# Optimization experiments

Measured on AMD Instinct MI355X. Metric: run time of the kernel, lower is better.

Reference implementation:

```python
import jax, jax.numpy as jnp
import numpy as np

THRESHOLD = 1.0
CURRENT_DECAY = 0.3
VOLTAGE_DECAY = 0.25
TAU_GRAD = 0.001  # surrogate-gradient sharpness (SLAYER escape-rate style)


@jax.custom_vjp
def spike(v):
    return (v >= THRESHOLD).astype(v.dtype)


def _spike_fwd(v):
    return spike(v), v


def _spike_bwd(v, g):
    # SLAYER-style surrogate: dS/dv = exp(-|v - theta| / tau) / tau
    return (g * jnp.exp(-jnp.abs(v - THRESHOLD) / TAU_GRAD) / TAU_GRAD,)


spike.defvjp(_spike_fwd, _spike_bwd)


def weight_norm(v, g):
    # torch weight_norm(dim=0): w = g * v / ||v|| with norm over all non-output dims
    axes = tuple(range(1, v.ndim))
    n = jnp.sqrt(jnp.sum(v * v, axis=axes, keepdims=True))
    return g.reshape((-1,) + (1,) * (v.ndim - 1)) * v / n


def cuba(z):
    # CUBA LIF dynamics over trailing time axis.  z: (B, ..., T)
    zt = jnp.moveaxis(z, -1, 0)  # (T, B, ...)

    def step(carry, z_t):
        c, v = carry
        c = (1.0 - CURRENT_DECAY) * c + z_t
        v = (1.0 - VOLTAGE_DECAY) * v + c
        s = spike(v)
        v = v * (1.0 - s)  # hard reset to zero on spike
        return (c, v), s

    init = (jnp.zeros_like(zt[0]), jnp.zeros_like(zt[0]))
    _, s = jax.lax.scan(step, init, zt)
    return jnp.moveaxis(s, 0, -1)  # (B, ..., T)


def conv2d_t(x, w):
    # Apply 2D conv independently per timestep. x: (B,C,H,W,T), w: (O,I,5,5)
    B, C, H, W, T = x.shape
    xb = jnp.moveaxis(x, -1, 1).reshape(B * T, C, H, W)
    y = jax.lax.conv_general_dilated(
        xb, w, window_strides=(4, 4), padding=[(1, 1), (1, 1)],
        dimension_numbers=('NCHW', 'OIHW', 'NCHW'))
    O, Ho, Wo = y.shape[1], y.shape[2], y.shape[3]
    return jnp.moveaxis(y.reshape(B, T, O, Ho, Wo), 1, -1)  # (B,O,Ho,Wo,T)


def dense_t(x, w):
    # x: (B, I, T), w: (O, I)
    return jnp.einsum('bit,oi->bot', x, w)


def setup_inputs() -> dict:
    key = jax.random.key(0)
    ks = jax.random.split(key, 8)
    B, T = 16, 64
    # sparse binary event input (DVS-like spikes)
    x = (jax.random.uniform(ks[0], (B, 2, 128, 128, T)) < 0.2).astype(jnp.float32)

    def mk(k, shape):
        fan_in = int(np.prod(shape[1:]))
        return jax.random.normal(k, shape, jnp.float32) / np.sqrt(fan_in)

    # weight_norm direction v; gain g absorbs weight_scale=2 (||w_eff|| = 2 per filter)
    return {
        'x': x,
        'conv1_v': mk(ks[1], (8, 2, 5, 5)),   'conv1_g': jnp.full((8,), 2.0, jnp.float32),
        'conv2_v': mk(ks[2], (32, 8, 5, 5)),  'conv2_g': jnp.full((32,), 2.0, jnp.float32),
        'conv3_v': mk(ks[3], (64, 32, 5, 5)), 'conv3_g': jnp.full((64,), 2.0, jnp.float32),
        'dense1_v': mk(ks[4], (2056, 256)),   'dense1_g': jnp.full((2056,), 2.0, jnp.float32),
        'dense2_v': mk(ks[5], (11, 2056)),    'dense2_g': jnp.full((11,), 2.0, jnp.float32),
    }


def reference(x, conv1_v, conv1_g, conv2_v, conv2_g, conv3_v, conv3_g,
              dense1_v, dense1_g, dense2_v, dense2_g):
    B = x.shape[0]
    T = x.shape[-1]
    # conv blocks: synapse then CUBA neuron
    for v, g in ((conv1_v, conv1_g), (conv2_v, conv2_g), (conv3_v, conv3_g)):
        x = cuba(conv2d_t(x, weight_norm(v, g)))
    # flatten (C,H,W) -> features; (B,64,2,2,T) -> (B,256,T)
    x = x.reshape(B, 64 * 2 * 2, T)
    for v, g in ((dense1_v, dense1_g), (dense2_v, dense2_g)):
        x = cuba(dense_t(x, weight_norm(v, g)))
    return x  # (B, 11, T) output spike train
```

## Files before the change

kernel.cpp:

```cpp
#include <hip/hip_runtime.h>
#include <cstddef>

#define TT 64

#define RFL(x) __builtin_amdgcn_readfirstlane(x)

__device__ __forceinline__ void scanc(float& c, float& v, float& z) {
    c = fmaf(0.7f, c, z);
    v = fmaf(0.75f, v, c);
    float s = (v >= 1.0f) ? 1.0f : 0.0f;
    v = (v >= 1.0f) ? 0.0f : v;
    z = s;
}
__device__ __forceinline__ void scan4(float& c, float& v, float4& a) {
    scanc(c, v, a.x); scanc(c, v, a.y); scanc(c, v, a.z); scanc(c, v, a.w);
}

__global__ __launch_bounds__(256) void wnorm_all(
    const float* __restrict__ c1v, const float* __restrict__ c1g, float* __restrict__ w1T,
    const float* __restrict__ c2v, const float* __restrict__ c2g, float* __restrict__ w2T,
    const float* __restrict__ c3v, const float* __restrict__ c3g, float* __restrict__ w3T,
    const float* __restrict__ d1v, const float* __restrict__ d1g, float* __restrict__ wd1,
    const float* __restrict__ d2v, const float* __restrict__ d2g, float* __restrict__ wd2P) {
    __shared__ float red[256];
    const int bid = blockIdx.x;
    const float *v, *g; float* w; int o, K, LD; bool tr;
    if (bid < 8)         { v = c1v; g = c1g; w = w1T;  o = bid;        K = 50;   LD = 8;  tr = true;  }
    else if (bid < 40)   { v = c2v; g = c2g; w = w2T;  o = bid - 8;    K = 200;  LD = 32; tr = true;  }
    else if (bid < 104)  { v = c3v; g = c3g; w = w3T;  o = bid - 40;   K = 800;  LD = 64; tr = true;  }
    else if (bid < 2160) { v = d1v; g = d1g; w = wd1;  o = bid - 104;  K = 256;  LD = 0;  tr = false; }
    else                 { v = d2v; g = d2g; w = wd2P; o = bid - 2160; K = 2056; LD = 12; tr = true;  }

    float s = 0.f;
    for (int k = threadIdx.x; k < K; k += 256) {
        float x = v[(size_t)o * K + k];
        s += x * x;
    }
    red[threadIdx.x] = s;
    __syncthreads();
    for (int off = 128; off > 0; off >>= 1) {
        if (threadIdx.x < off) red[threadIdx.x] += red[threadIdx.x + off];
        __syncthreads();
    }
    const float scale = g[o] / sqrtf(red[0]);
    for (int k = threadIdx.x; k < K; k += 256) {
        float val = scale * v[(size_t)o * K + k];
        if (tr) w[(size_t)k * LD + o] = val;
        else    w[(size_t)o * K + k] = val;
    }
}

__global__ __launch_bounds__(256) void conv1_cuba(const float* __restrict__ x,
                                                  const float* __restrict__ w1T,
                                                  float* __restrict__ s1) {
    __shared__ float lds[4][8][68];
    const int wid = RFL(threadIdx.x >> 6), t = threadIdx.x & 63;
    const int task = RFL(blockIdx.x) * 4 + wid;
    const int spi = task & 1023, b = task >> 10;
    const int oy = spi >> 5, ox = spi & 31;

    float a0=0,a1=0,a2=0,a3=0,a4=0,a5=0,a6=0,a7=0;
    const float* xb = x + (size_t)b * 2 * 128 * 128 * TT + t;

    if (oy >= 1 && ox >= 1) {
        const float* xq = xb + ((size_t)((oy * 4 - 1) * 128 + ox * 4 - 1)) * TT;
        float xv[50];
#pragma unroll
        for (int ci = 0; ci < 2; ci++)
#pragma unroll
            for (int ky = 0; ky < 5; ky++)
#pragma unroll
                for (int kx = 0; kx < 5; kx++)
                    xv[ci * 25 + ky * 5 + kx] =
                        xq[((size_t)(ci * 16384 + ky * 128 + kx)) * TT];
#pragma unroll
        for (int k = 0; k < 50; k++) {
            const float4* wp = (const float4*)(w1T + k * 8);
            const float4 wA = wp[0], wB = wp[1];
            const float xvk = xv[k];
            a0 = fmaf(wA.x, xvk, a0); a1 = fmaf(wA.y, xvk, a1);
            a2 = fmaf(wA.z, xvk, a2); a3 = fmaf(wA.w, xvk, a3);
            a4 = fmaf(wB.x, xvk, a4); a5 = fmaf(wB.y, xvk, a5);
            a6 = fmaf(wB.z, xvk, a6); a7 = fmaf(wB.w, xvk, a7);
        }
    } else {
        for (int ci = 0; ci < 2; ci++) {
#pragma unroll
            for (int ky = 0; ky < 5; ky++) {
                const int iy = oy * 4 + ky - 1;
                if (iy < 0 || iy >= 128) continue;
#pragma unroll
                for (int kx = 0; kx < 5; kx++) {
                    const int ix = ox * 4 + kx - 1;
                    if (ix < 0 || ix >= 128) continue;
                    const float xvk = xb[((size_t)((ci * 128 + iy) * 128 + ix)) * TT];
                    const float4* wp = (const float4*)(w1T + (ci * 25 + ky * 5 + kx) * 8);
                    const float4 wA = wp[0], wB = wp[1];
                    a0 = fmaf(wA.x, xvk, a0); a1 = fmaf(wA.y, xvk, a1);
                    a2 = fmaf(wA.z, xvk, a2); a3 = fmaf(wA.w, xvk, a3);
                    a4 = fmaf(wB.x, xvk, a4); a5 = fmaf(wB.y, xvk, a5);
                    a6 = fmaf(wB.z, xvk, a6); a7 = fmaf(wB.w, xvk, a7);
                }
            }
        }
    }
    lds[wid][0][t] = a0; lds[wid][1][t] = a1; lds[wid][2][t] = a2; lds[wid][3][t] = a3;
    lds[wid][4][t] = a4; lds[wid][5][t] = a5; lds[wid][6][t] = a6; lds[wid][7][t] = a7;
    __syncthreads();
    if (t < 8) {
        const float* row = &lds[wid][t][0];
        float4* op = (float4*)(s1 + (((size_t)b * 8 + t) * 1024 + spi) * TT);
        float c = 0.f, v = 0.f;
        for (int tc = 0; tc < 4; tc++) {
            float4 r0 = *(const float4*)&row[tc * 16 + 0];
            float4 r1 = *(const float4*)&row[tc * 16 + 4];
            float4 r2 = *(const float4*)&row[tc * 16 + 8];
            float4 r3 = *(const float4*)&row[tc * 16 + 12];
            scan4(c, v, r0); scan4(c, v, r1); scan4(c, v, r2); scan4(c, v, r3);
            op[tc * 4 + 0] = r0; op[tc * 4 + 1] = r1;
            op[tc * 4 + 2] = r2; op[tc * 4 + 3] = r3;
        }
    }
}

__global__ __launch_bounds__(256) void conv2_cuba(const float* __restrict__ s1,
                                                  const float* __restrict__ w2T,
                                                  float* __restrict__ s2) {
    __shared__ float lds[4][16][68];
    const int wid = RFL(threadIdx.x >> 6), t = threadIdx.x & 63;
    const int task = RFL(blockIdx.x) * 4 + wid;
    const int og = task & 1;
    const int spi = (task >> 1) & 63;
    const int b = task >> 7;
    const int oy = spi >> 3, ox = spi & 7;

    float a[16];
#pragma unroll
    for (int j = 0; j < 16; j++) a[j] = 0.f;
    const float* xb = s1 + (size_t)b * 8 * 32 * 32 * TT + t;

    if (oy >= 1 && ox >= 1) {
        const float* xq = xb + ((size_t)((oy * 4 - 1) * 32 + ox * 4 - 1)) * TT;
        for (int cp = 0; cp < 4; cp++) {
            float xv[50];
#pragma unroll
            for (int cc = 0; cc < 2; cc++)
#pragma unroll
                for (int ky = 0; ky < 5; ky++)
#pragma unroll
                    for (int kx = 0; kx < 5; kx++)
                        xv[cc * 25 + ky * 5 + kx] =
                            xq[((size_t)(((cp * 2 + cc) * 1024) + ky * 32 + kx)) * TT];
#pragma unroll
            for (int k = 0; k < 50; k++) {
                const int row = (cp * 2 + (k >= 25 ? 1 : 0)) * 25 + (k >= 25 ? k - 25 : k);
                const float4* wp = (const float4*)(w2T + row * 32 + og * 16);
                const float4 w0 = wp[0], w1 = wp[1], w2 = wp[2], w3 = wp[3];
                const float xvk = xv[k];
                a[0]  = fmaf(w0.x, xvk, a[0]);  a[1]  = fmaf(w0.y, xvk, a[1]);
                a[2]  = fmaf(w0.z, xvk, a[2]);  a[3]  = fmaf(w0.w, xvk, a[3]);
                a[4]  = fmaf(w1.x, xvk, a[4]);  a[5]  = fmaf(w1.y, xvk, a[5]);
                a[6]  = fmaf(w1.z, xvk, a[6]);  a[7]  = fmaf(w1.w, xvk, a[7]);
                a[8]  = fmaf(w2.x, xvk, a[8]);  a[9]  = fmaf(w2.y, xvk, a[9]);
                a[10] = fmaf(w2.z, xvk, a[10]); a[11] = fmaf(w2.w, xvk, a[11]);
                a[12] = fmaf(w3.x, xvk, a[12]); a[13] = fmaf(w3.y, xvk, a[13]);
                a[14] = fmaf(w3.z, xvk, a[14]); a[15] = fmaf(w3.w, xvk, a[15]);
            }
        }
    } else {
        for (int ci = 0; ci < 8; ci++) {
#pragma unroll
            for (int ky = 0; ky < 5; ky++) {
                const int iy = oy * 4 + ky - 1;
                if (iy < 0 || iy >= 32) continue;
#pragma unroll
                for (int kx = 0; kx < 5; kx++) {
                    const int ix = ox * 4 + kx - 1;
                    if (ix < 0 || ix >= 32) continue;
                    const float xvk = xb[((size_t)((ci * 32 + iy) * 32 + ix)) * TT];
                    const float4* wp =
                        (const float4*)(w2T + (ci * 25 + ky * 5 + kx) * 32 + og * 16);
                    const float4 w0 = wp[0], w1 = wp[1], w2 = wp[2], w3 = wp[3];
                    a[0]  = fmaf(w0.x, xvk, a[0]);  a[1]  = fmaf(w0.y, xvk, a[1]);
                    a[2]  = fmaf(w0.z, xvk, a[2]);  a[3]  = fmaf(w0.w, xvk, a[3]);
                    a[4]  = fmaf(w1.x, xvk, a[4]);  a[5]  = fmaf(w1.y, xvk, a[5]);
                    a[6]  = fmaf(w1.z, xvk, a[6]);  a[7]  = fmaf(w1.w, xvk, a[7]);
                    a[8]  = fmaf(w2.x, xvk, a[8]);  a[9]  = fmaf(w2.y, xvk, a[9]);
                    a[10] = fmaf(w2.z, xvk, a[10]); a[11] = fmaf(w2.w, xvk, a[11]);
                    a[12] = fmaf(w3.x, xvk, a[12]); a[13] = fmaf(w3.y, xvk, a[13]);
                    a[14] = fmaf(w3.z, xvk, a[14]); a[15] = fmaf(w3.w, xvk, a[15]);
                }
            }
        }
    }
#pragma unroll
    for (int j = 0; j < 16; j++) lds[wid][j][t] = a[j];
    __syncthreads();
    if (t < 16) {
        const float* row = &lds[wid][t][0];
        float4* op = (float4*)(s2 + (((size_t)b * 32 + og * 16 + t) * 64 + spi) * TT);
        float c = 0.f, v = 0.f;
        for (int tc = 0; tc < 4; tc++) {
            float4 r0 = *(const float4*)&row[tc * 16 + 0];
            float4 r1 = *(const float4*)&row[tc * 16 + 4];
            float4 r2 = *(const float4*)&row[tc * 16 + 8];
            float4 r3 = *(const float4*)&row[tc * 16 + 12];
            scan4(c, v, r0); scan4(c, v, r1); scan4(c, v, r2); scan4(c, v, r3);
            op[tc * 4 + 0] = r0; op[tc * 4 + 1] = r1;
            op[tc * 4 + 2] = r2; op[tc * 4 + 3] = r3;
        }
    }
}

template <int OY, int OX>
__device__ __forceinline__ void conv3_acc(const float* __restrict__ xb,
                                          const float* __restrict__ wTo,
                                          int wid, float* __restrict__ acc) {
    constexpr int KY0 = (OY == 0) ? 1 : 0;
    constexpr int KX0 = (OX == 0) ? 1 : 0;
    constexpr int NKY = 5 - KY0;
    constexpr int NKX = 5 - KX0;
    for (int c8 = 0; c8 < 8; c8++) {
        const int ci = wid * 8 + c8;
        float xv[NKY * NKX];
#pragma unroll
        for (int ky = KY0; ky < 5; ky++) {
#pragma unroll
            for (int kx = KX0; kx < 5; kx++) {
                const int iy = OY * 4 + ky - 1;
                const int ix = OX * 4 + kx - 1;
                xv[(ky - KY0) * NKX + (kx - KX0)] =
                    xb[((size_t)((ci * 8 + iy) * 8 + ix)) * TT];
            }
        }
#pragma unroll
        for (int ky = KY0; ky < 5; ky++) {
#pragma unroll
            for (int kx = KX0; kx < 5; kx++) {
                const float xvk = xv[(ky - KY0) * NKX + (kx - KX0)];
                const float4* wp = (const float4*)(wTo + (ci * 25 + ky * 5 + kx) * 64);
                const float4 wA = wp[0], wB = wp[1];
                acc[0] = fmaf(wA.x, xvk, acc[0]); acc[1] = fmaf(wA.y, xvk, acc[1]);
                acc[2] = fmaf(wA.z, xvk, acc[2]); acc[3] = fmaf(wA.w, xvk, acc[3]);
                acc[4] = fmaf(wB.x, xvk, acc[4]); acc[5] = fmaf(wB.y, xvk, acc[5]);
                acc[6] = fmaf(wB.z, xvk, acc[6]); acc[7] = fmaf(wB.w, xvk, acc[7]);
            }
        }
    }
}

__global__ __launch_bounds__(256) void conv3_cuba(const float* __restrict__ s2,
                                                  const float* __restrict__ wT,
                                                  float* __restrict__ s3) {
    __shared__ float red[4][8][68];
    const int wid = RFL(threadIdx.x >> 6), t = threadIdx.x & 63;
    const int og = RFL(blockIdx.x) & 7;
    const int spi = (RFL(blockIdx.x) >> 3) & 3;
    const int b = RFL(blockIdx.x) >> 5;

    float acc[8];
#pragma unroll
    for (int j = 0; j < 8; j++) acc[j] = 0.f;
    const float* xb = s2 + (size_t)b * 32 * 8 * 8 * TT + t;
    const float* wTo = wT + og * 8;

    switch (spi) {
        case 0: conv3_acc<0, 0>(xb, wTo, wid, acc); break;
        case 1: conv3_acc<0, 1>(xb, wTo, wid, acc); break;
        case 2: conv3_acc<1, 0>(xb, wTo, wid, acc); break;
        default: conv3_acc<1, 1>(xb, wTo, wid, acc); break;
    }
#pragma unroll
    for (int j = 0; j < 8; j++) red[wid][j][t] = acc[j];
    __syncthreads();
    if (wid == 0) {
#pragma unroll
        for (int j = 0; j < 8; j++)
            red[0][j][t] = ((red[0][j][t] + red[1][j][t]) + red[2][j][t]) + red[3][j][t];
    }
    __syncthreads();
    if (threadIdx.x < 8) {
        const int j = threadIdx.x;
        const float* row = &red[0][j][0];
        float4* op = (float4*)(s3 + ((size_t)b * 256 + og * 32 + j * 4 + spi) * TT);
        float c = 0.f, v = 0.f;
        for (int tc = 0; tc < 4; tc++) {
            float4 r0 = *(const float4*)&row[tc * 16 + 0];
            float4 r1 = *(const float4*)&row[tc * 16 + 4];
            float4 r2 = *(const float4*)&row[tc * 16 + 8];
            float4 r3 = *(const float4*)&row[tc * 16 + 12];
            scan4(c, v, r0); scan4(c, v, r1); scan4(c, v, r2); scan4(c, v, r3);
            op[tc * 4 + 0] = r0; op[tc * 4 + 1] = r1;
            op[tc * 4 + 2] = r2; op[tc * 4 + 3] = r3;
        }
    }
}

__global__ __launch_bounds__(256) void dense1_cuba(const float* __restrict__ s3,
                                                   const float* __restrict__ w,
                                                   float* __restrict__ s4) {
    __shared__ float lds[4][8][68];
    const int wid = threadIdx.x >> 6, t = threadIdx.x & 63;
    const int task = blockIdx.x * 4 + wid;
    const int bq = task / 257;
    const int ogq = task - bq * 257;
    const int b = RFL(bq);
    const int o0 = RFL(ogq * 8);

    float a0=0,a1=0,a2=0,a3=0,a4=0,a5=0,a6=0,a7=0;
    const float* ab = s3 + (size_t)b * 256 * TT + t;
    const float* r0 = w + (size_t)(o0 + 0) * 256;
    const float* r1 = w + (size_t)(o0 + 1) * 256;
    const float* r2 = w + (size_t)(o0 + 2) * 256;
    const float* r3 = w + (size_t)(o0 + 3) * 256;
    const float* r4 = w + (size_t)(o0 + 4) * 256;
    const float* r5 = w + (size_t)(o0 + 5) * 256;
    const float* r6 = w + (size_t)(o0 + 6) * 256;
    const float* r7 = w + (size_t)(o0 + 7) * 256;

#pragma unroll 2
    for (int i = 0; i < 256; i += 4) {
        const float av0 = ab[(size_t)(i + 0) * TT];
        const float av1 = ab[(size_t)(i + 1) * TT];
        const float av2 = ab[(size_t)(i + 2) * TT];
        const float av3 = ab[(size_t)(i + 3) * TT];
        const float4 q0 = *(const float4*)(r0 + i);
        const float4 q1 = *(const float4*)(r1 + i);
        const float4 q2 = *(const float4*)(r2 + i);
        const float4 q3 = *(const float4*)(r3 + i);
        const float4 q4 = *(const float4*)(r4 + i);
        const float4 q5 = *(const float4*)(r5 + i);
        const float4 q6 = *(const float4*)(r6 + i);
        const float4 q7 = *(const float4*)(r7 + i);
        a0 = fmaf(q0.x, av0, a0); a1 = fmaf(q1.x, av0, a1);
        a2 = fmaf(q2.x, av0, a2); a3 = fmaf(q3.x, av0, a3);
        a4 = fmaf(q4.x, av0, a4); a5 = fmaf(q5.x, av0, a5);
        a6 = fmaf(q6.x, av0, a6); a7 = fmaf(q7.x, av0, a7);
        a0 = fmaf(q0.y, av1, a0); a1 = fmaf(q1.y, av1, a1);
        a2 = fmaf(q2.y, av1, a2); a3 = fmaf(q3.y, av1, a3);
        a4 = fmaf(q4.y, av1, a4); a5 = fmaf(q5.y, av1, a5);
        a6 = fmaf(q6.y, av1, a6); a7 = fmaf(q7.y, av1, a7);
        a0 = fmaf(q0.z, av2, a0); a1 = fmaf(q1.z, av2, a1);
        a2 = fmaf(q2.z, av2, a2); a3 = fmaf(q3.z, av2, a3);
        a4 = fmaf(q4.z, av2, a4); a5 = fmaf(q5.z, av2, a5);
        a6 = fmaf(q6.z, av2, a6); a7 = fmaf(q7.z, av2, a7);
        a0 = fmaf(q0.w, av3, a0); a1 = fmaf(q1.w, av3, a1);
        a2 = fmaf(q2.w, av3, a2); a3 = fmaf(q3.w, av3, a3);
        a4 = fmaf(q4.w, av3, a4); a5 = fmaf(q5.w, av3, a5);
        a6 = fmaf(q6.w, av3, a6); a7 = fmaf(q7.w, av3, a7);
    }
    lds[wid][0][t] = a0; lds[wid][1][t] = a1; lds[wid][2][t] = a2; lds[wid][3][t] = a3;
    lds[wid][4][t] = a4; lds[wid][5][t] = a5; lds[wid][6][t] = a6; lds[wid][7][t] = a7;
    __syncthreads();
    if (t < 8) {
        const float* row = &lds[wid][t][0];
        float4* op = (float4*)(s4 + ((size_t)b * 2056 + o0 + t) * TT);
        float c = 0.f, v = 0.f;
        for (int tc = 0; tc < 4; tc++) {
            float4 r0q = *(const float4*)&row[tc * 16 + 0];
            float4 r1q = *(const float4*)&row[tc * 16 + 4];
            float4 r2q = *(const float4*)&row[tc * 16 + 8];
            float4 r3q = *(const float4*)&row[tc * 16 + 12];
            scan4(c, v, r0q); scan4(c, v, r1q); scan4(c, v, r2q); scan4(c, v, r3q);
            op[tc * 4 + 0] = r0q; op[tc * 4 + 1] = r1q;
            op[tc * 4 + 2] = r2q; op[tc * 4 + 3] = r3q;
        }
    }
}

__global__ __launch_bounds__(256) void dense2_part(const float* __restrict__ s4,
                                                   const float* __restrict__ wP,
                                                   float* __restrict__ z4p) {
    __shared__ float red[4][11][64];
    const int sp = blockIdx.x, b = blockIdx.y;
    const int w = threadIdx.x >> 6, t = threadIdx.x & 63;
    const int i0 = sp * 257, iend = i0 + 257;
    const float* src = s4 + (size_t)b * 2056 * TT + t;

    float acc[11];
#pragma unroll
    for (int j = 0; j < 11; j++) acc[j] = 0.f;

    for (int i = i0 + w; i < iend; i += 4) {
        const float xv = src[(size_t)i * TT];
        const float4* wp = (const float4*)(wP + (size_t)i * 12);
        const float4 w0 = wp[0], w1 = wp[1], w2 = wp[2];
        acc[0]  = fmaf(w0.x, xv, acc[0]);  acc[1]  = fmaf(w0.y, xv, acc[1]);
        acc[2]  = fmaf(w0.z, xv, acc[2]);  acc[3]  = fmaf(w0.w, xv, acc[3]);
        acc[4]  = fmaf(w1.x, xv, acc[4]);  acc[5]  = fmaf(w1.y, xv, acc[5]);
        acc[6]  = fmaf(w1.z, xv, acc[6]);  acc[7]  = fmaf(w1.w, xv, acc[7]);
        acc[8]  = fmaf(w2.x, xv, acc[8]);  acc[9]  = fmaf(w2.y, xv, acc[9]);
        acc[10] = fmaf(w2.z, xv, acc[10]);
    }
#pragma unroll
    for (int j = 0; j < 11; j++) red[w][j][t] = acc[j];
    __syncthreads();
    if (w == 0) {
#pragma unroll
        for (int j = 0; j < 11; j++) {
            const float s = red[0][j][t] + red[1][j][t] + red[2][j][t] + red[3][j][t];
            z4p[(((size_t)b * 8 + sp) * 11 + j) * TT + t] = s;
        }
    }
}

__global__ __launch_bounds__(256) void dense2_scan(const float* __restrict__ z4p,
                                                   float* __restrict__ out) {
    __shared__ float z[11][64];
    const int b = blockIdx.x;
    for (int idx = threadIdx.x; idx < 11 * 64; idx += 256) {
        const int o = idx >> 6, t = idx & 63;
        float s = 0.f;
#pragma unroll
        for (int sp = 0; sp < 8; sp++)
            s += z4p[(((size_t)b * 8 + sp) * 11 + o) * TT + t];
        z[o][t] = s;
    }
    __syncthreads();
    if (threadIdx.x < 11) {
        const int o = threadIdx.x;
        float c = 0.f, v = 0.f;
        float* op = out + ((size_t)b * 11 + o) * TT;
#pragma unroll
        for (int t = 0; t < TT; t++) {
            float zz = z[o][t];
            scanc(c, v, zz);
            op[t] = zz;
        }
    }
}

extern "C" void kernel_launch(void* const* d_in, const int* in_sizes, int n_in,
                              void* d_out, int out_size, void* d_ws, size_t ws_size,
                              hipStream_t stream) {
    const float* x   = (const float*)d_in[0];
    const float* c1v = (const float*)d_in[1];  const float* c1g = (const float*)d_in[2];
    const float* c2v = (const float*)d_in[3];  const float* c2g = (const float*)d_in[4];
    const float* c3v = (const float*)d_in[5];  const float* c3g = (const float*)d_in[6];
    const float* d1v = (const float*)d_in[7];  const float* d1g = (const float*)d_in[8];
    const float* d2v = (const float*)d_in[9];  const float* d2g = (const float*)d_in[10];

    float* ws = (float*)d_ws;
    float* w1T  = ws + 0;
    float* w2T  = ws + 400;
    float* w3T  = ws + 6800;
    float* wd1  = ws + 58000;
    float* wd2P = ws + 584336;
    float* A = ws + 609008;
    float* B = A + 8388608;
    float* s1  = A;
    float* s3  = A;
    float* s4  = A + 262144;
    float* s2  = B;
    float* z4p = B + 2097152;
    (void)ws_size; (void)in_sizes; (void)n_in; (void)out_size;

    wnorm_all<<<dim3(2171), dim3(256), 0, stream>>>(c1v, c1g, w1T, c2v, c2g, w2T,
                                                    c3v, c3g, w3T, d1v, d1g, wd1,
                                                    d2v, d2g, wd2P);

    conv1_cuba <<<dim3(4096), dim3(256), 0, stream>>>(x, w1T, s1);
    conv2_cuba <<<dim3(512),  dim3(256), 0, stream>>>(s1, w2T, s2);
    conv3_cuba <<<dim3(512),  dim3(256), 0, stream>>>(s2, w3T, s3);
    dense1_cuba<<<dim3(1028), dim3(256), 0, stream>>>(s3, wd1, s4);
    dense2_part<<<dim3(8, 16), dim3(256), 0, stream>>>(s4, wd2P, z4p);
    dense2_scan<<<dim3(16),   dim3(256), 0, stream>>>(z4p, (float*)d_out);
}
```

Before: 163.4 us.

## Bit-pack binary input and conv1 spikes into 64-bit time masks

Adds a pack_x kernel that ballots the binary input over the 64 timesteps into one u64 per pixel, and makes conv1 emit its output spikes as u64 masks. conv1 and conv2 now read these masks and extract each lane's bit, so the 5x5 window costs far fewer loads. The pack kernel still has to read the full 134MB float input once, so the saving depends on how many times conv1 reloaded the overlapping windows. It assumes the input is exactly 0/1 (threshold 0.5), which matches the binary spike semantics.

New measurement: 197.0 us. 20.6% more time.

```diff
diff --git a/kernel.cpp b/kernel.cpp
--- a/kernel.cpp
+++ b/kernel.cpp
@@ -4,6 +4,8 @@
 #define TT 64
 
 #define RFL(x) __builtin_amdgcn_readfirstlane(x)
+
+typedef unsigned long long u64;
 
 __device__ __forceinline__ void scanc(float& c, float& v, float& z) {
     c = fmaf(0.7f, c, z);
@@ -14,6 +16,9 @@
 }
 __device__ __forceinline__ void scan4(float& c, float& v, float4& a) {
     scanc(c, v, a.x); scanc(c, v, a.y); scanc(c, v, a.z); scanc(c, v, a.w);
+}
+__device__ __forceinline__ float bit2f(u64 m, int t) {
+    return (float)((m >> t) & 1ULL);
 }
 
 __global__ __launch_bounds__(256) void wnorm_all(
@@ -50,9 +55,18 @@
     }
 }
 
-__global__ __launch_bounds__(256) void conv1_cuba(const float* __restrict__ x,
+__global__ __launch_bounds__(256) void pack_x(const float* __restrict__ x,
+                                              u64* __restrict__ xb) {
+    const int wid = threadIdx.x >> 6, t = threadIdx.x & 63;
+    const size_t p = (size_t)blockIdx.x * 4 + wid;
+    const float v = x[p * TT + t];
+    const u64 m = __ballot(v > 0.5f);
+    if (t == 0) xb[p] = m;
+}
+
+__global__ __launch_bounds__(256) void conv1_cuba(const u64* __restrict__ xb,
                                                   const float* __restrict__ w1T,
-                                                  float* __restrict__ s1) {
+                                                  u64* __restrict__ s1b) {
     __shared__ float lds[4][8][68];
     const int wid = RFL(threadIdx.x >> 6), t = threadIdx.x & 63;
     const int task = RFL(blockIdx.x) * 4 + wid;
@@ -60,28 +74,27 @@
     const int oy = spi >> 5, ox = spi & 31;
 
     float a0=0,a1=0,a2=0,a3=0,a4=0,a5=0,a6=0,a7=0;
-    const float* xb = x + (size_t)b * 2 * 128 * 128 * TT + t;
+    const u64* xq = xb + (size_t)b * 2 * 16384;
 
     if (oy >= 1 && ox >= 1) {
-        const float* xq = xb + ((size_t)((oy * 4 - 1) * 128 + ox * 4 - 1)) * TT;
-        float xv[50];
-#pragma unroll
-        for (int ci = 0; ci < 2; ci++)
+        const u64* xi = xq + (size_t)(oy * 4 - 1) * 128 + (ox * 4 - 1);
+        for (int ci = 0; ci < 2; ci++) {
+            u64 m[25];
 #pragma unroll
             for (int ky = 0; ky < 5; ky++)
 #pragma unroll
                 for (int kx = 0; kx < 5; kx++)
-                    xv[ci * 25 + ky * 5 + kx] =
-                        xq[((size_t)(ci * 16384 + ky * 128 + kx)) * TT];
-#pragma unroll
-        for (int k = 0; k < 50; k++) {
-            const float4* wp = (const float4*)(w1T + k * 8);
-            const float4 wA = wp[0], wB = wp[1];
-            const float xvk = xv[k];
-            a0 = fmaf(wA.x, xvk, a0); a1 = fmaf(wA.y, xvk, a1);
-            a2 = fmaf(wA.z, xvk, a2); a3 = fmaf(wA.w, xvk, a3);
-            a4 = fmaf(wB.x, xvk, a4); a5 = fmaf(wB.y, xvk, a5);
-            a6 = fmaf(wB.z, xvk, a6); a7 = fmaf(wB.w, xvk, a7);
+                    m[ky * 5 + kx] = xi[ci * 16384 + ky * 128 + kx];
+#pragma unroll
+            for (int k = 0; k < 25; k++) {
+                const float xvk = bit2f(m[k], t);
+                const float4* wp = (const float4*)(w1T + (ci * 25 + k) * 8);
+                const float4 wA = wp[0], wB = wp[1];
+                a0 = fmaf(wA.x, xvk, a0); a1 = fmaf(wA.y, xvk, a1);
+                a2 = fmaf(wA.z, xvk, a2); a3 = fmaf(wA.w, xvk, a3);
+                a4 = fmaf(wB.x, xvk, a4); a5 = fmaf(wB.y, xvk, a5);
+                a6 = fmaf(wB.z, xvk, a6); a7 = fmaf(wB.w, xvk, a7);
+            }
         }
     } else {
         for (int ci = 0; ci < 2; ci++) {
@@ -93,7 +106,7 @@
                 for (int kx = 0; kx < 5; kx++) {
                     const int ix = ox * 4 + kx - 1;
                     if (ix < 0 || ix >= 128) continue;
-                    const float xvk = xb[((size_t)((ci * 128 + iy) * 128 + ix)) * TT];
+                    const float xvk = bit2f(xq[ci * 16384 + iy * 128 + ix], t);
                     const float4* wp = (const float4*)(w1T + (ci * 25 + ky * 5 + kx) * 8);
                     const float4 wA = wp[0], wB = wp[1];
                     a0 = fmaf(wA.x, xvk, a0); a1 = fmaf(wA.y, xvk, a1);
@@ -108,8 +121,7 @@
     lds[wid][4][t] = a4; lds[wid][5][t] = a5; lds[wid][6][t] = a6; lds[wid][7][t] = a7;
     __syncthreads();
     if (t < 8) {
-        const float* row = &lds[wid][t][0];
-        float4* op = (float4*)(s1 + (((size_t)b * 8 + t) * 1024 + spi) * TT);
+        float* row = &lds[wid][t][0];
         float c = 0.f, v = 0.f;
         for (int tc = 0; tc < 4; tc++) {
             float4 r0 = *(const float4*)&row[tc * 16 + 0];
@@ -117,13 +129,20 @@
             float4 r2 = *(const float4*)&row[tc * 16 + 8];
             float4 r3 = *(const float4*)&row[tc * 16 + 12];
             scan4(c, v, r0); scan4(c, v, r1); scan4(c, v, r2); scan4(c, v, r3);
-            op[tc * 4 + 0] = r0; op[tc * 4 + 1] = r1;
-            op[tc * 4 + 2] = r2; op[tc * 4 + 3] = r3;
-        }
-    }
-}
-
-__global__ __launch_bounds__(256) void conv2_cuba(const float* __restrict__ s1,
+            *(float4*)&row[tc * 16 + 0] = r0; *(float4*)&row[tc * 16 + 4] = r1;
+            *(float4*)&row[tc * 16 + 8] = r2; *(float4*)&row[tc * 16 + 12] = r3;
+        }
+    }
+    __syncthreads();
+    u64* ob = s1b + (size_t)b * 8 * 1024 + spi;
+#pragma unroll
+    for (int ch = 0; ch < 8; ch++) {
+        const u64 m = __ballot(lds[wid][ch][t] > 0.5f);
+        if (t == 0) ob[(size_t)ch * 1024] = m;
+    }
+}
+
+__global__ __launch_bounds__(256) void conv2_cuba(const u64* __restrict__ s1b,
                                                   const float* __restrict__ w2T,
                                                   float* __restrict__ s2) {
     __shared__ float lds[4][16][68];
@@ -137,26 +156,22 @@
     float a[16];
 #pragma unroll
     for (int j = 0; j < 16; j++) a[j] = 0.f;
-    const float* xb = s1 + (size_t)b * 8 * 32 * 32 * TT + t;
+    const u64* sb = s1b + (size_t)b * 8 * 1024;
 
     if (oy >= 1 && ox >= 1) {
-        const float* xq = xb + ((size_t)((oy * 4 - 1) * 32 + ox * 4 - 1)) * TT;
-        for (int cp = 0; cp < 4; cp++) {
-            float xv[50];
-#pragma unroll
-            for (int cc = 0; cc < 2; cc++)
-#pragma unroll
-                for (int ky = 0; ky < 5; ky++)
-#pragma unroll
-                    for (int kx = 0; kx < 5; kx++)
-                        xv[cc * 25 + ky * 5 + kx] =
-                            xq[((size_t)(((cp * 2 + cc) * 1024) + ky * 32 + kx)) * TT];
-#pragma unroll
-            for (int k = 0; k < 50; k++) {
-                const int row = (cp * 2 + (k >= 25 ? 1 : 0)) * 25 + (k >= 25 ? k - 25 : k);
-                const float4* wp = (const float4*)(w2T + row * 32 + og * 16);
+        const u64* si = sb + (size_t)(oy * 4 - 1) * 32 + (ox * 4 - 1);
+        for (int ci = 0; ci < 8; ci++) {
+            u64 m[25];
+#pragma unroll
+            for (int ky = 0; ky < 5; ky++)
+#pragma unroll
+                for (int kx = 0; kx < 5; kx++)
+                    m[ky * 5 + kx] = si[ci * 1024 + ky * 32 + kx];
+#pragma unroll
+            for (int k = 0; k < 25; k++) {
+                const float xvk = bit2f(m[k], t);
+                const float4* wp = (const float4*)(w2T + (ci * 25 + k) * 32 + og * 16);
                 const float4 w0 = wp[0], w1 = wp[1], w2 = wp[2], w3 = wp[3];
-                const float xvk = xv[k];
                 a[0]  = fmaf(w0.x, xvk, a[0]);  a[1]  = fmaf(w0.y, xvk, a[1]);
                 a[2]  = fmaf(w0.z, xvk, a[2]);  a[3]  = fmaf(w0.w, xvk, a[3]);
                 a[4]  = fmaf(w1.x, xvk, a[4]);  a[5]  = fmaf(w1.y, xvk, a[5]);
@@ -177,7 +192,7 @@
                 for (int kx = 0; kx < 5; kx++) {
                     const int ix = ox * 4 + kx - 1;
                     if (ix < 0 || ix >= 32) continue;
-                    const float xvk = xb[((size_t)((ci * 32 + iy) * 32 + ix)) * TT];
+                    const float xvk = bit2f(sb[ci * 1024 + iy * 32 + ix], t);
                     const float4* wp =
                         (const float4*)(w2T + (ci * 25 + ky * 5 + kx) * 32 + og * 16);
                     const float4 w0 = wp[0], w1 = wp[1], w2 = wp[2], w3 = wp[3];
@@ -448,19 +463,21 @@
     float* wd2P = ws + 584336;
     float* A = ws + 609008;
     float* B = A + 8388608;
-    float* s1  = A;
     float* s3  = A;
     float* s4  = A + 262144;
     float* s2  = B;
     float* z4p = B + 2097152;
+    u64* xbits  = (u64*)(ws + 13191920);
+    u64* s1bits = (u64*)(ws + 14240496);
     (void)ws_size; (void)in_sizes; (void)n_in; (void)out_size;
 
     wnorm_all<<<dim3(2171), dim3(256), 0, stream>>>(c1v, c1g, w1T, c2v, c2g, w2T,
                                                     c3v, c3g, w3T, d1v, d1g, wd1,
                                                     d2v, d2g, wd2P);
-
-    conv1_cuba <<<dim3(4096), dim3(256), 0, stream>>>(x, w1T, s1);
-    conv2_cuba <<<dim3(512),  dim3(256), 0, stream>>>(s1, w2T, s2);
+    pack_x<<<dim3(131072), dim3(256), 0, stream>>>(x, xbits);
+
+    conv1_cuba <<<dim3(4096), dim3(256), 0, stream>>>(xbits, w1T, s1bits);
+    conv2_cuba <<<dim3(512),  dim3(256), 0, stream>>>(s1bits, w2T, s2);
     conv3_cuba <<<dim3(512),  dim3(256), 0, stream>>>(s2, w3T, s3);
     dense1_cuba<<<dim3(1028), dim3(256), 0, stream>>>(s3, wd1, s4);
     dense2_part<<<dim3(8, 16), dim3(256), 0, stream>>>(s4, wd2P, z4p);
```
